# Kernel tuning notes

Measured on AMD Instinct MI355X. Metric: run time of the kernel, lower is better.

## Reference

```python
import jax, jax.numpy as jnp
import numpy as np

PI = float(np.pi)
CUTOFF = 10.0
SLOPE = 0.015  # LeakyReLU negative slope

N_NODES = 50000
N_EDGES = 1600000
HIDDEN = 128
FILTERS = 128
GAUSSIANS = 50


def _leaky(x):
    return jnp.where(x >= 0, x, SLOPE * x)


def setup_inputs() -> dict:
    key = jax.random.key(0)
    ks = jax.random.split(key, 10)

    def xavier(k, shape):
        fan_in, fan_out = shape[1], shape[0]
        a = float(np.sqrt(6.0 / (fan_in + fan_out)))
        return jax.random.uniform(k, shape, jnp.float32, -a, a)

    v = jax.random.normal(ks[0], (N_NODES, HIDDEN), jnp.float32)
    dist = jax.random.uniform(ks[1], (N_EDGES,), jnp.float32)  # in [0,1) < cutoff
    dist_emb = jax.random.normal(ks[2], (N_EDGES, GAUSSIANS), jnp.float32)
    edge_index = jax.random.randint(ks[3], (2, N_EDGES), 0, N_NODES, jnp.int64)

    return {
        "v": v,
        "dist": dist,
        "dist_emb": dist_emb,
        "edge_index": edge_index,
        "lin_w": xavier(ks[4], (FILTERS, HIDDEN)),          # Linear(hidden->filters), no bias
        "mlp_w1": xavier(ks[5], (FILTERS, GAUSSIANS)),
        "mlp_b1": jnp.zeros((FILTERS,), jnp.float32),
        "mlp_w2": xavier(ks[6], (FILTERS, FILTERS)),
        "mlp_b2": jnp.zeros((FILTERS,), jnp.float32),
        "mlp_w3": xavier(ks[7], (FILTERS, FILTERS)),
        "mlp_b3": jnp.zeros((FILTERS,), jnp.float32),
        "lin_out_w": xavier(ks[8], (FILTERS, FILTERS)),
        "lin_out_b": jnp.zeros((FILTERS,), jnp.float32),
    }


def reference(v, dist, dist_emb, edge_index, lin_w, mlp_w1, mlp_b1,
              mlp_w2, mlp_b2, mlp_w3, mlp_b3, lin_out_w, lin_out_b):
    j = edge_index[0]
    # cosine cutoff: [E]
    C = 0.5 * (jnp.cos(dist * (PI / CUTOFF)) + 1.0)
    # filter MLP on gaussian basis: [E, F]
    h = _leaky(dist_emb @ mlp_w1.T + mlp_b1)
    h = _leaky(h @ mlp_w2.T + mlp_b2)
    W = (h @ mlp_w3.T + mlp_b3) * C[:, None]
    # project node features, gather source nodes, multiply by filter
    vp = v @ lin_w.T          # [N, F]
    e = vp[j] * W             # [E, F]
    return e @ lin_out_w.T + lin_out_b + e
```

## Files before the change

kernel.cpp:

```cpp
#include <hip/hip_runtime.h>
#include <math.h>

typedef __attribute__((ext_vector_type(8))) short short8;
typedef __attribute__((ext_vector_type(4))) float f32x4;
typedef __attribute__((ext_vector_type(2))) float f32x2;
typedef __attribute__((ext_vector_type(4))) unsigned u32x4;

#define PI_OVER_CUTOFF 0.31415926535897932f
#define SLOPE 0.015f

__device__ __forceinline__ unsigned short f2bf(float x) {
    unsigned u = __float_as_uint(x);
    return (unsigned short)((u + 0x7FFFu + ((u >> 16) & 1u)) >> 16);
}
__device__ __forceinline__ unsigned cvt_pk_bf16(float lo, float hi) {
    unsigned r;
    asm("v_cvt_pk_bf16_f32 %0, %1, %2" : "=v"(r) : "v"(lo), "v"(hi));
    return r;
}
__device__ __forceinline__ short8 pack4(unsigned a, unsigned b, unsigned c, unsigned d) {
    u32x4 t = {a, b, c, d};
    return __builtin_bit_cast(short8, t);
}
__device__ __forceinline__ short8 mulbf8(short8 w, short8 v) {
    u32x4 uw = __builtin_bit_cast(u32x4, w);
    u32x4 uv = __builtin_bit_cast(u32x4, v);
    unsigned r0, r1, r2, r3;
#define MB(i, r)                                                         \
    {                                                                    \
        float wl = __uint_as_float(uw[i] << 16);                         \
        float wh = __uint_as_float(uw[i] & 0xFFFF0000u);                 \
        float vl = __uint_as_float(uv[i] << 16);                         \
        float vh = __uint_as_float(uv[i] & 0xFFFF0000u);                 \
        r = cvt_pk_bf16(wl * vl, wh * vh);                               \
    }
    MB(0, r0) MB(1, r1) MB(2, r2) MB(3, r3)
#undef MB
    return pack4(r0, r1, r2, r3);
}

#define GLOAD_LDS16(g, l)                                                                      \
    __builtin_amdgcn_global_load_lds((const __attribute__((address_space(1))) unsigned*)(g),   \
                                     (__attribute__((address_space(3))) unsigned*)(l), 16, 0, 0)

__global__ void prep_weights(const float* __restrict__ w1, const float* __restrict__ w2,
                             const float* __restrict__ w3, const float* __restrict__ wo,
                             unsigned short* __restrict__ w1s, unsigned short* __restrict__ w2s,
                             unsigned short* __restrict__ w3s, unsigned short* __restrict__ wos) {
    int i = blockIdx.x * 256 + threadIdx.x;
    if (i < 128 * 128) {
        int c = i >> 7, k = i & 127;
        int d = c * 128 + (k ^ ((c & 15) << 3));
        w1s[d] = (k < 50) ? f2bf(w1[c * 50 + k]) : (unsigned short)0;
        w2s[d] = f2bf(w2[i]);
        w3s[d] = f2bf(w3[i]);
        wos[d] = f2bf(wo[i] + ((c == k) ? 1.0f : 0.0f));
    }
}

__global__ __launch_bounds__(256) void vp_gemm(const float* __restrict__ v,
                                               const float* __restrict__ lin_w,
                                               unsigned short* __restrict__ vp, int nnodes) {
    const int tid = threadIdx.x;
    const int lane = tid & 63;
    const int wv = tid >> 6;
    const int l15 = lane & 15;
    const int l4 = lane >> 4;
    const int r0 = blockIdx.x * 64;
    const int c0 = wv * 32;

    f32x4 acc[4][2] = {};
#pragma unroll
    for (int kf = 0; kf < 4; ++kf) {
        short8 a[4];
#pragma unroll
        for (int mf = 0; mf < 4; ++mf) {
            int row = r0 + mf * 16 + l15;
            f32x4 x0 = {}, x1 = {};
            if (row < nnodes) {
                const float* p = v + (size_t)row * 128 + kf * 32 + l4 * 8;
                x0 = *reinterpret_cast<const f32x4*>(p);
                x1 = *reinterpret_cast<const f32x4*>(p + 4);
            }
            a[mf] = pack4(cvt_pk_bf16(x0[0], x0[1]), cvt_pk_bf16(x0[2], x0[3]),
                          cvt_pk_bf16(x1[0], x1[1]), cvt_pk_bf16(x1[2], x1[3]));
        }
        short8 b[2];
#pragma unroll
        for (int nf = 0; nf < 2; ++nf) {
            const float* p = lin_w + (size_t)(c0 + nf * 16 + l15) * 128 + kf * 32 + l4 * 8;
            f32x4 x0 = *reinterpret_cast<const f32x4*>(p);
            f32x4 x1 = *reinterpret_cast<const f32x4*>(p + 4);
            b[nf] = pack4(cvt_pk_bf16(x0[0], x0[1]), cvt_pk_bf16(x0[2], x0[3]),
                          cvt_pk_bf16(x1[0], x1[1]), cvt_pk_bf16(x1[2], x1[3]));
        }
#pragma unroll
        for (int mf = 0; mf < 4; ++mf)
#pragma unroll
            for (int nf = 0; nf < 2; ++nf)
                acc[mf][nf] = __builtin_amdgcn_mfma_f32_16x16x32_bf16(a[mf], b[nf], acc[mf][nf], 0, 0, 0);
    }
#pragma unroll
    for (int mf = 0; mf < 4; ++mf)
#pragma unroll
        for (int nf = 0; nf < 2; ++nf)
#pragma unroll
            for (int q = 0; q < 4; ++q) {
                int row = r0 + mf * 16 + l4 * 4 + q;
                if (row < nnodes)
                    vp[(size_t)row * 128 + c0 + nf * 16 + l15] = f2bf(acc[mf][nf][q]);
            }
}

__global__ __launch_bounds__(256, 1) void fused_edge(
    const float* __restrict__ dist, const float* __restrict__ dist_emb,
    const int* __restrict__ edge_index,
    const float* __restrict__ b1, const float* __restrict__ b2,
    const float* __restrict__ b3, const float* __restrict__ bo,
    const unsigned short* __restrict__ vp,
    const unsigned short* __restrict__ w1s, const unsigned short* __restrict__ w2s,
    const unsigned short* __restrict__ w3s, const unsigned short* __restrict__ wos,
    float* __restrict__ out) {
    __shared__ __align__(16) unsigned char lds_h[4][16384];
    __shared__ __align__(16) unsigned short wbuf[2][16384];

    const int tid = threadIdx.x;
    const int lane = tid & 63;
    const int wv = tid >> 6;
    const int l15 = lane & 15;
    const int l4 = lane >> 4;
    const long e0 = (long)blockIdx.x * 256 + wv * 64;
    unsigned char* hb = lds_h[wv];

#define STAGE_W(src, buf)                                                  \
    _Pragma("unroll")                                                      \
    for (int it = 0; it < 8; ++it) {                                       \
        int chunk = it * 4 + wv;                                           \
        GLOAD_LDS16((src) + chunk * 512 + lane * 8, &wbuf[buf][chunk * 512]); \
    }

    STAGE_W(w1s, 0)
    STAGE_W(w2s, 1)

    int jm[4];
#pragma unroll
    for (int mf = 0; mf < 4; ++mf)
        jm[mf] = edge_index[e0 + mf * 16 + l15] * 128;
    float bb1[8], bb2[8], bb3[8], bbo[8];
#pragma unroll
    for (int nf = 0; nf < 8; ++nf) {
        bb1[nf] = b1[nf * 16 + l15];
        bb2[nf] = b2[nf * 16 + l15];
        bb3[nf] = b3[nf * 16 + l15];
        bbo[nf] = bo[nf * 16 + l15];
    }

    f32x4 acc[4][8];

#define EPILOGUE_TO_LDS()                                                           \
    _Pragma("unroll")                                                               \
    for (int mf = 0; mf < 4; ++mf)                                                  \
        _Pragma("unroll")                                                           \
        for (int nf = 0; nf < 8; ++nf) {                                            \
            f32x4 vv = acc[mf][nf];                                                 \
            _Pragma("unroll")                                                       \
            for (int q = 0; q < 4; ++q) vv[q] = fmaxf(vv[q], SLOPE * vv[q]);        \
            unsigned p01 = cvt_pk_bf16(vv[0], vv[1]);                               \
            unsigned p23 = cvt_pk_bf16(vv[2], vv[3]);                               \
            int col2 = (nf * 16 + l15) * 2;                                         \
            int rb = mf * 16 + l4 * 4;                                              \
            *(unsigned short*)(hb + (rb + 0) * 256 + (col2 ^ ((l4 * 4 + 0) << 4))) = (unsigned short)p01;         \
            *(unsigned short*)(hb + (rb + 1) * 256 + (col2 ^ ((l4 * 4 + 1) << 4))) = (unsigned short)(p01 >> 16); \
            *(unsigned short*)(hb + (rb + 2) * 256 + (col2 ^ ((l4 * 4 + 2) << 4))) = (unsigned short)p23;         \
            *(unsigned short*)(hb + (rb + 3) * 256 + (col2 ^ ((l4 * 4 + 3) << 4))) = (unsigned short)(p23 >> 16); \
        }

#define HB_READ(mf, kf) \
    (*reinterpret_cast<const short8*>(hb + ((mf) * 16 + l15) * 256 + (((kf) * 64 + l4 * 16) ^ (l15 << 4))))
#define WB_READ(buf, nf, kf) \
    (*reinterpret_cast<const short8*>(&wbuf[buf][((nf) * 16 + l15) * 128 + (((kf) * 32 + l4 * 8) ^ (l15 << 3))]))

    __syncthreads();

#pragma unroll
    for (int nf = 0; nf < 8; ++nf) {
        float b = bb1[nf];
#pragma unroll
        for (int mf = 0; mf < 4; ++mf) acc[mf][nf] = (f32x4){b, b, b, b};
    }
#pragma unroll
    for (int kf = 0; kf < 2; ++kf) {
        short8 a[4];
#pragma unroll
        for (int mf = 0; mf < 4; ++mf) {
            const float* src = dist_emb + (e0 + mf * 16 + l15) * 50 + kf * 32 + l4 * 8;
            unsigned pk[4];
#pragma unroll
            for (int p = 0; p < 4; ++p) {
                int k2 = kf * 32 + l4 * 8 + 2 * p;
                f32x2 x = (k2 < 50) ? *reinterpret_cast<const f32x2*>(src + 2 * p)
                                    : (f32x2){0.f, 0.f};
                pk[p] = cvt_pk_bf16(x[0], x[1]);
            }
            a[mf] = pack4(pk[0], pk[1], pk[2], pk[3]);
        }
#pragma unroll
        for (int nf = 0; nf < 8; ++nf) {
            short8 b = WB_READ(0, nf, kf);
#pragma unroll
            for (int mf = 0; mf < 4; ++mf)
                acc[mf][nf] = __builtin_amdgcn_mfma_f32_16x16x32_bf16(a[mf], b, acc[mf][nf], 0, 0, 0);
        }
    }
    EPILOGUE_TO_LDS()

    __syncthreads();
    STAGE_W(w3s, 0)

#pragma unroll
    for (int nf = 0; nf < 8; ++nf) {
        float b = bb2[nf];
#pragma unroll
        for (int mf = 0; mf < 4; ++mf) acc[mf][nf] = (f32x4){b, b, b, b};
    }
#pragma unroll
    for (int kf = 0; kf < 4; ++kf) {
        short8 a[4];
#pragma unroll
        for (int mf = 0; mf < 4; ++mf) a[mf] = HB_READ(mf, kf);
#pragma unroll
        for (int nf = 0; nf < 8; ++nf) {
            short8 b = WB_READ(1, nf, kf);
#pragma unroll
            for (int mf = 0; mf < 4; ++mf)
                acc[mf][nf] = __builtin_amdgcn_mfma_f32_16x16x32_bf16(a[mf], b, acc[mf][nf], 0, 0, 0);
        }
    }
    EPILOGUE_TO_LDS()

    __syncthreads();
    STAGE_W(wos, 1)

    {
        short8 vpr[4][4];
#pragma unroll
        for (int mf = 0; mf < 4; ++mf)
#pragma unroll
            for (int kf = 0; kf < 4; ++kf)
                vpr[mf][kf] = *reinterpret_cast<const short8*>(vp + jm[mf] + kf * 32 + l4 * 8);

        float dd[4][4];
#pragma unroll
        for (int mf = 0; mf < 4; ++mf)
#pragma unroll
            for (int q = 0; q < 4; ++q)
                dd[mf][q] = dist[e0 + mf * 16 + l4 * 4 + q];

#pragma unroll
        for (int nf = 0; nf < 8; ++nf) {
            float b = bb3[nf];
#pragma unroll
            for (int mf = 0; mf < 4; ++mf) acc[mf][nf] = (f32x4){b, b, b, b};
        }
#pragma unroll
        for (int kf = 0; kf < 4; ++kf) {
            short8 a[4];
#pragma unroll
            for (int mf = 0; mf < 4; ++mf) a[mf] = HB_READ(mf, kf);
#pragma unroll
            for (int nf = 0; nf < 8; ++nf) {
                short8 b = WB_READ(0, nf, kf);
#pragma unroll
                for (int mf = 0; mf < 4; ++mf)
                    acc[mf][nf] = __builtin_amdgcn_mfma_f32_16x16x32_bf16(a[mf], b, acc[mf][nf], 0, 0, 0);
            }
        }
        float Cw[4][4];
#pragma unroll
        for (int mf = 0; mf < 4; ++mf)
#pragma unroll
            for (int q = 0; q < 4; ++q)
                Cw[mf][q] = 0.5f * (__cosf(dd[mf][q] * PI_OVER_CUTOFF) + 1.0f);
#pragma unroll
        for (int mf = 0; mf < 4; ++mf)
#pragma unroll
            for (int nf = 0; nf < 8; ++nf) {
                f32x4 vv = acc[mf][nf];
#pragma unroll
                for (int q = 0; q < 4; ++q) vv[q] = vv[q] * Cw[mf][q];
                unsigned p01 = cvt_pk_bf16(vv[0], vv[1]);
                unsigned p23 = cvt_pk_bf16(vv[2], vv[3]);
                int col2 = (nf * 16 + l15) * 2;
                int rb = mf * 16 + l4 * 4;
                *(unsigned short*)(hb + (rb + 0) * 256 + (col2 ^ ((l4 * 4 + 0) << 4))) = (unsigned short)p01;
                *(unsigned short*)(hb + (rb + 1) * 256 + (col2 ^ ((l4 * 4 + 1) << 4))) = (unsigned short)(p01 >> 16);
                *(unsigned short*)(hb + (rb + 2) * 256 + (col2 ^ ((l4 * 4 + 2) << 4))) = (unsigned short)p23;
                *(unsigned short*)(hb + (rb + 3) * 256 + (col2 ^ ((l4 * 4 + 3) << 4))) = (unsigned short)(p23 >> 16);
            }

        __syncthreads();

#pragma unroll
        for (int nf = 0; nf < 8; ++nf) {
            float b = bbo[nf];
#pragma unroll
            for (int mf = 0; mf < 4; ++mf) acc[mf][nf] = (f32x4){b, b, b, b};
        }
#pragma unroll
        for (int kf = 0; kf < 4; ++kf) {
            short8 a[4];
#pragma unroll
            for (int mf = 0; mf < 4; ++mf) a[mf] = mulbf8(HB_READ(mf, kf), vpr[mf][kf]);
#pragma unroll
            for (int nf = 0; nf < 8; ++nf) {
                short8 b = WB_READ(1, nf, kf);
#pragma unroll
                for (int mf = 0; mf < 4; ++mf)
                    acc[mf][nf] = __builtin_amdgcn_mfma_f32_16x16x32_bf16(a[mf], b, acc[mf][nf], 0, 0, 0);
            }
        }
        float* op = out + (size_t)e0 * 128;
#pragma unroll
        for (int mf = 0; mf < 4; ++mf)
#pragma unroll
            for (int nf = 0; nf < 8; ++nf)
#pragma unroll
                for (int q = 0; q < 4; ++q)
                    op[(size_t)(mf * 16 + l4 * 4 + q) * 128 + nf * 16 + l15] = acc[mf][nf][q];
    }
#undef EPILOGUE_TO_LDS
#undef HB_READ
#undef WB_READ
#undef STAGE_W
}

extern "C" void kernel_launch(void* const* d_in, const int* in_sizes, int n_in,
                              void* d_out, int out_size, void* d_ws, size_t ws_size,
                              hipStream_t stream) {
    const float* v        = (const float*)d_in[0];
    const float* dist     = (const float*)d_in[1];
    const float* dist_emb = (const float*)d_in[2];
    const int*   edge_idx = (const int*)d_in[3];
    const float* lin_w    = (const float*)d_in[4];
    const float* w1 = (const float*)d_in[5];
    const float* b1 = (const float*)d_in[6];
    const float* w2 = (const float*)d_in[7];
    const float* b2 = (const float*)d_in[8];
    const float* w3 = (const float*)d_in[9];
    const float* b3 = (const float*)d_in[10];
    const float* wo = (const float*)d_in[11];
    const float* bo = (const float*)d_in[12];
    float* out = (float*)d_out;

    const int nnodes = in_sizes[0] / 128;
    const int E = in_sizes[1];

    unsigned short* vp  = (unsigned short*)d_ws;
    unsigned short* w1s = vp + (size_t)nnodes * 128;
    unsigned short* w2s = w1s + 128 * 128;
    unsigned short* w3s = w2s + 128 * 128;
    unsigned short* wos = w3s + 128 * 128;

    prep_weights<<<64, 256, 0, stream>>>(w1, w2, w3, wo, w1s, w2s, w3s, wos);
    vp_gemm<<<(nnodes + 63) / 64, 256, 0, stream>>>(v, lin_w, vp, nnodes);
    fused_edge<<<E / 256, 256, 0, stream>>>(dist, dist_emb, edge_idx,
                                            b1, b2, b3, bo, vp,
                                            w1s, w2s, w3s, wos, out);
}
```

Measured before the change: 526.5 us.

## Split each wave's 64 edges into two 32-row halves to cut accumulator registers

Each wave now processes its 64 edges as two sequential 32-row halves, with separate LDS regions h0 and h1. This halves the accumulator array from 4x8 to 2x8 f32x4. The dist_emb loads for both halves are hoisted to the top of the kernel, and the vp gathers for each half are issued just before that half's layer-3 GEMM. The goal is to lower VGPR pressure and possible spills and to overlap global loads with MFMA work. The cost is that each weight fragment read from LDS now feeds two MFMAs instead of four, which doubles B-operand LDS traffic per MFMA.

```diff
diff --git a/kernel.cpp b/kernel.cpp
--- a/kernel.cpp
+++ b/kernel.cpp
@@ -130,7 +130,8 @@
     const int l15 = lane & 15;
     const int l4 = lane >> 4;
     const long e0 = (long)blockIdx.x * 256 + wv * 64;
-    unsigned char* hb = lds_h[wv];
+    unsigned char* h0 = lds_h[wv];
+    unsigned char* h1 = lds_h[wv] + 8192;
 
 #define STAGE_W(src, buf)                                                  \
     _Pragma("unroll")                                                      \
@@ -142,10 +143,26 @@
     STAGE_W(w1s, 0)
     STAGE_W(w2s, 1)
 
-    int jm[4];
-#pragma unroll
-    for (int mf = 0; mf < 4; ++mf)
-        jm[mf] = edge_index[e0 + mf * 16 + l15] * 128;
+    short8 ea[2][2], eb[2][2];
+#define LOAD_EMB(E, OFS)                                                            \
+    _Pragma("unroll")                                                               \
+    for (int mf = 0; mf < 2; ++mf)                                                  \
+        _Pragma("unroll")                                                           \
+        for (int kf = 0; kf < 2; ++kf) {                                            \
+            const float* src = dist_emb + (e0 + (OFS) + mf * 16 + l15) * 50 + kf * 32 + l4 * 8; \
+            unsigned pk[4];                                                         \
+            _Pragma("unroll")                                                       \
+            for (int p = 0; p < 4; ++p) {                                           \
+                int k2 = kf * 32 + l4 * 8 + 2 * p;                                  \
+                f32x2 x = (k2 < 50) ? *reinterpret_cast<const f32x2*>(src + 2 * p)  \
+                                    : (f32x2){0.f, 0.f};                            \
+                pk[p] = cvt_pk_bf16(x[0], x[1]);                                    \
+            }                                                                       \
+            E[mf][kf] = pack4(pk[0], pk[1], pk[2], pk[3]);                          \
+        }
+    LOAD_EMB(ea, 0)
+    LOAD_EMB(eb, 32)
+
     float bb1[8], bb2[8], bb3[8], bbo[8];
 #pragma unroll
     for (int nf = 0; nf < 8; ++nf) {
@@ -155,11 +172,24 @@
         bbo[nf] = bo[nf * 16 + l15];
     }
 
-    f32x4 acc[4][8];
-
-#define EPILOGUE_TO_LDS()                                                           \
-    _Pragma("unroll")                                                               \
-    for (int mf = 0; mf < 4; ++mf)                                                  \
+    f32x4 acc[2][8];
+
+#define WB_READ(buf, nf, kf) \
+    (*reinterpret_cast<const short8*>(&wbuf[buf][((nf) * 16 + l15) * 128 + (((kf) * 32 + l4 * 8) ^ (l15 << 3))]))
+#define HB_READ(H, mf, kf) \
+    (*reinterpret_cast<const short8*>((H) + ((mf) * 16 + l15) * 256 + (((kf) * 64 + l4 * 16) ^ (l15 << 4))))
+
+#define INIT_ACC(bb)                                                                \
+    _Pragma("unroll")                                                               \
+    for (int nf = 0; nf < 8; ++nf) {                                                \
+        float b = (bb)[nf];                                                         \
+        acc[0][nf] = (f32x4){b, b, b, b};                                           \
+        acc[1][nf] = acc[0][nf];                                                    \
+    }
+
+#define EPILOGUE_TO(H)                                                              \
+    _Pragma("unroll")                                                               \
+    for (int mf = 0; mf < 2; ++mf)                                                  \
         _Pragma("unroll")                                                           \
         for (int nf = 0; nf < 8; ++nf) {                                            \
             f32x4 vv = acc[mf][nf];                                                 \
@@ -169,168 +199,155 @@
             unsigned p23 = cvt_pk_bf16(vv[2], vv[3]);                               \
             int col2 = (nf * 16 + l15) * 2;                                         \
             int rb = mf * 16 + l4 * 4;                                              \
-            *(unsigned short*)(hb + (rb + 0) * 256 + (col2 ^ ((l4 * 4 + 0) << 4))) = (unsigned short)p01;         \
-            *(unsigned short*)(hb + (rb + 1) * 256 + (col2 ^ ((l4 * 4 + 1) << 4))) = (unsigned short)(p01 >> 16); \
-            *(unsigned short*)(hb + (rb + 2) * 256 + (col2 ^ ((l4 * 4 + 2) << 4))) = (unsigned short)p23;         \
-            *(unsigned short*)(hb + (rb + 3) * 256 + (col2 ^ ((l4 * 4 + 3) << 4))) = (unsigned short)(p23 >> 16); \
+            *(unsigned short*)((H) + (rb + 0) * 256 + (col2 ^ ((l4 * 4 + 0) << 4))) = (unsigned short)p01;         \
+            *(unsigned short*)((H) + (rb + 1) * 256 + (col2 ^ ((l4 * 4 + 1) << 4))) = (unsigned short)(p01 >> 16); \
+            *(unsigned short*)((H) + (rb + 2) * 256 + (col2 ^ ((l4 * 4 + 2) << 4))) = (unsigned short)p23;         \
+            *(unsigned short*)((H) + (rb + 3) * 256 + (col2 ^ ((l4 * 4 + 3) << 4))) = (unsigned short)(p23 >> 16); \
         }
 
-#define HB_READ(mf, kf) \
-    (*reinterpret_cast<const short8*>(hb + ((mf) * 16 + l15) * 256 + (((kf) * 64 + l4 * 16) ^ (l15 << 4))))
-#define WB_READ(buf, nf, kf) \
-    (*reinterpret_cast<const short8*>(&wbuf[buf][((nf) * 16 + l15) * 128 + (((kf) * 32 + l4 * 8) ^ (l15 << 3))]))
+#define S1_BODY(E, H)                                                               \
+    INIT_ACC(bb1)                                                                   \
+    _Pragma("unroll")                                                               \
+    for (int kf = 0; kf < 2; ++kf) {                                                \
+        _Pragma("unroll")                                                           \
+        for (int nf = 0; nf < 8; ++nf) {                                            \
+            short8 b = WB_READ(0, nf, kf);                                          \
+            acc[0][nf] = __builtin_amdgcn_mfma_f32_16x16x32_bf16(E[0][kf], b, acc[0][nf], 0, 0, 0); \
+            acc[1][nf] = __builtin_amdgcn_mfma_f32_16x16x32_bf16(E[1][kf], b, acc[1][nf], 0, 0, 0); \
+        }                                                                           \
+    }                                                                               \
+    EPILOGUE_TO(H)
+
+#define S2_BODY(H, BUF, BB)                                                         \
+    INIT_ACC(BB)                                                                    \
+    _Pragma("unroll")                                                               \
+    for (int kf = 0; kf < 4; ++kf) {                                                \
+        short8 a0 = HB_READ(H, 0, kf);                                              \
+        short8 a1 = HB_READ(H, 1, kf);                                              \
+        _Pragma("unroll")                                                           \
+        for (int nf = 0; nf < 8; ++nf) {                                            \
+            short8 b = WB_READ(BUF, nf, kf);                                        \
+            acc[0][nf] = __builtin_amdgcn_mfma_f32_16x16x32_bf16(a0, b, acc[0][nf], 0, 0, 0); \
+            acc[1][nf] = __builtin_amdgcn_mfma_f32_16x16x32_bf16(a1, b, acc[1][nf], 0, 0, 0); \
+        }                                                                           \
+    }
+
+#define S3_EPI(H, DD)                                                               \
+    {                                                                               \
+        float Cw[2][4];                                                             \
+        _Pragma("unroll")                                                           \
+        for (int mf = 0; mf < 2; ++mf)                                              \
+            _Pragma("unroll")                                                       \
+            for (int q = 0; q < 4; ++q)                                             \
+                Cw[mf][q] = 0.5f * (__cosf(DD[mf][q] * PI_OVER_CUTOFF) + 1.0f);     \
+        _Pragma("unroll")                                                           \
+        for (int mf = 0; mf < 2; ++mf)                                              \
+            _Pragma("unroll")                                                       \
+            for (int nf = 0; nf < 8; ++nf) {                                        \
+                f32x4 vv = acc[mf][nf];                                             \
+                _Pragma("unroll")                                                   \
+                for (int q = 0; q < 4; ++q) vv[q] = vv[q] * Cw[mf][q];              \
+                unsigned p01 = cvt_pk_bf16(vv[0], vv[1]);                           \
+                unsigned p23 = cvt_pk_bf16(vv[2], vv[3]);                           \
+                int col2 = (nf * 16 + l15) * 2;                                     \
+                int rb = mf * 16 + l4 * 4;                                          \
+                *(unsigned short*)((H) + (rb + 0) * 256 + (col2 ^ ((l4 * 4 + 0) << 4))) = (unsigned short)p01;         \
+                *(unsigned short*)((H) + (rb + 1) * 256 + (col2 ^ ((l4 * 4 + 1) << 4))) = (unsigned short)(p01 >> 16); \
+                *(unsigned short*)((H) + (rb + 2) * 256 + (col2 ^ ((l4 * 4 + 2) << 4))) = (unsigned short)p23;         \
+                *(unsigned short*)((H) + (rb + 3) * 256 + (col2 ^ ((l4 * 4 + 3) << 4))) = (unsigned short)(p23 >> 16); \
+            }                                                                       \
+    }
+
+#define S4_BODY(H, V, OFS)                                                          \
+    INIT_ACC(bbo)                                                                   \
+    _Pragma("unroll")                                                               \
+    for (int kf = 0; kf < 4; ++kf) {                                                \
+        short8 a0 = mulbf8(HB_READ(H, 0, kf), V[0][kf]);                            \
+        short8 a1 = mulbf8(HB_READ(H, 1, kf), V[1][kf]);                            \
+        _Pragma("unroll")                                                           \
+        for (int nf = 0; nf < 8; ++nf) {                                            \
+            short8 b = WB_READ(1, nf, kf);                                          \
+            acc[0][nf] = __builtin_amdgcn_mfma_f32_16x16x32_bf16(a0, b, acc[0][nf], 0, 0, 0); \
+            acc[1][nf] = __builtin_amdgcn_mfma_f32_16x16x32_bf16(a1, b, acc[1][nf], 0, 0, 0); \
+        }                                                                           \
+    }                                                                               \
+    {                                                                               \
+        float* op = out + (size_t)(e0 + (OFS)) * 128;                               \
+        _Pragma("unroll")                                                           \
+        for (int mf = 0; mf < 2; ++mf)                                              \
+            _Pragma("unroll")                                                       \
+            for (int nf = 0; nf < 8; ++nf)                                          \
+                _Pragma("unroll")                                                   \
+                for (int q = 0; q < 4; ++q)                                         \
+                    op[(size_t)(mf * 16 + l4 * 4 + q) * 128 + nf * 16 + l15] = acc[mf][nf][q]; \
+    }
 
     __syncthreads();
 
-#pragma unroll
-    for (int nf = 0; nf < 8; ++nf) {
-        float b = bb1[nf];
-#pragma unroll
-        for (int mf = 0; mf < 4; ++mf) acc[mf][nf] = (f32x4){b, b, b, b};
-    }
-#pragma unroll
-    for (int kf = 0; kf < 2; ++kf) {
-        short8 a[4];
-#pragma unroll
-        for (int mf = 0; mf < 4; ++mf) {
-            const float* src = dist_emb + (e0 + mf * 16 + l15) * 50 + kf * 32 + l4 * 8;
-            unsigned pk[4];
-#pragma unroll
-            for (int p = 0; p < 4; ++p) {
-                int k2 = kf * 32 + l4 * 8 + 2 * p;
-                f32x2 x = (k2 < 50) ? *reinterpret_cast<const f32x2*>(src + 2 * p)
-                                    : (f32x2){0.f, 0.f};
-                pk[p] = cvt_pk_bf16(x[0], x[1]);
-            }
-            a[mf] = pack4(pk[0], pk[1], pk[2], pk[3]);
-        }
-#pragma unroll
-        for (int nf = 0; nf < 8; ++nf) {
-            short8 b = WB_READ(0, nf, kf);
-#pragma unroll
-            for (int mf = 0; mf < 4; ++mf)
-                acc[mf][nf] = __builtin_amdgcn_mfma_f32_16x16x32_bf16(a[mf], b, acc[mf][nf], 0, 0, 0);
-        }
-    }
-    EPILOGUE_TO_LDS()
+    S1_BODY(ea, h0)
+    S1_BODY(eb, h1)
 
     __syncthreads();
     STAGE_W(w3s, 0)
 
-#pragma unroll
-    for (int nf = 0; nf < 8; ++nf) {
-        float b = bb2[nf];
-#pragma unroll
-        for (int mf = 0; mf < 4; ++mf) acc[mf][nf] = (f32x4){b, b, b, b};
-    }
-#pragma unroll
-    for (int kf = 0; kf < 4; ++kf) {
-        short8 a[4];
-#pragma unroll
-        for (int mf = 0; mf < 4; ++mf) a[mf] = HB_READ(mf, kf);
-#pragma unroll
-        for (int nf = 0; nf < 8; ++nf) {
-            short8 b = WB_READ(1, nf, kf);
-#pragma unroll
-            for (int mf = 0; mf < 4; ++mf)
-                acc[mf][nf] = __builtin_amdgcn_mfma_f32_16x16x32_bf16(a[mf], b, acc[mf][nf], 0, 0, 0);
-        }
-    }
-    EPILOGUE_TO_LDS()
+    S2_BODY(h0, 1, bb2)
+    EPILOGUE_TO(h0)
+    S2_BODY(h1, 1, bb2)
+    EPILOGUE_TO(h1)
 
     __syncthreads();
     STAGE_W(wos, 1)
 
-    {
-        short8 vpr[4][4];
-#pragma unroll
-        for (int mf = 0; mf < 4; ++mf)
-#pragma unroll
-            for (int kf = 0; kf < 4; ++kf)
-                vpr[mf][kf] = *reinterpret_cast<const short8*>(vp + jm[mf] + kf * 32 + l4 * 8);
-
-        float dd[4][4];
-#pragma unroll
-        for (int mf = 0; mf < 4; ++mf)
-#pragma unroll
-            for (int q = 0; q < 4; ++q)
-                dd[mf][q] = dist[e0 + mf * 16 + l4 * 4 + q];
-
-#pragma unroll
-        for (int nf = 0; nf < 8; ++nf) {
-            float b = bb3[nf];
-#pragma unroll
-            for (int mf = 0; mf < 4; ++mf) acc[mf][nf] = (f32x4){b, b, b, b};
-        }
-#pragma unroll
-        for (int kf = 0; kf < 4; ++kf) {
-            short8 a[4];
-#pragma unroll
-            for (int mf = 0; mf < 4; ++mf) a[mf] = HB_READ(mf, kf);
-#pragma unroll
-            for (int nf = 0; nf < 8; ++nf) {
-                short8 b = WB_READ(0, nf, kf);
-#pragma unroll
-                for (int mf = 0; mf < 4; ++mf)
-                    acc[mf][nf] = __builtin_amdgcn_mfma_f32_16x16x32_bf16(a[mf], b, acc[mf][nf], 0, 0, 0);
-            }
-        }
-        float Cw[4][4];
-#pragma unroll
-        for (int mf = 0; mf < 4; ++mf)
-#pragma unroll
-            for (int q = 0; q < 4; ++q)
-                Cw[mf][q] = 0.5f * (__cosf(dd[mf][q] * PI_OVER_CUTOFF) + 1.0f);
-#pragma unroll
-        for (int mf = 0; mf < 4; ++mf)
-#pragma unroll
-            for (int nf = 0; nf < 8; ++nf) {
-                f32x4 vv = acc[mf][nf];
-#pragma unroll
-                for (int q = 0; q < 4; ++q) vv[q] = vv[q] * Cw[mf][q];
-                unsigned p01 = cvt_pk_bf16(vv[0], vv[1]);
-                unsigned p23 = cvt_pk_bf16(vv[2], vv[3]);
-                int col2 = (nf * 16 + l15) * 2;
-                int rb = mf * 16 + l4 * 4;
-                *(unsigned short*)(hb + (rb + 0) * 256 + (col2 ^ ((l4 * 4 + 0) << 4))) = (unsigned short)p01;
-                *(unsigned short*)(hb + (rb + 1) * 256 + (col2 ^ ((l4 * 4 + 1) << 4))) = (unsigned short)(p01 >> 16);
-                *(unsigned short*)(hb + (rb + 2) * 256 + (col2 ^ ((l4 * 4 + 2) << 4))) = (unsigned short)p23;
-                *(unsigned short*)(hb + (rb + 3) * 256 + (col2 ^ ((l4 * 4 + 3) << 4))) = (unsigned short)(p23 >> 16);
-            }
-
-        __syncthreads();
-
-#pragma unroll
-        for (int nf = 0; nf < 8; ++nf) {
-            float b = bbo[nf];
-#pragma unroll
-            for (int mf = 0; mf < 4; ++mf) acc[mf][nf] = (f32x4){b, b, b, b};
-        }
-#pragma unroll
-        for (int kf = 0; kf < 4; ++kf) {
-            short8 a[4];
-#pragma unroll
-            for (int mf = 0; mf < 4; ++mf) a[mf] = mulbf8(HB_READ(mf, kf), vpr[mf][kf]);
-#pragma unroll
-            for (int nf = 0; nf < 8; ++nf) {
-                short8 b = WB_READ(1, nf, kf);
-#pragma unroll
-                for (int mf = 0; mf < 4; ++mf)
-                    acc[mf][nf] = __builtin_amdgcn_mfma_f32_16x16x32_bf16(a[mf], b, acc[mf][nf], 0, 0, 0);
-            }
-        }
-        float* op = out + (size_t)e0 * 128;
-#pragma unroll
-        for (int mf = 0; mf < 4; ++mf)
-#pragma unroll
-            for (int nf = 0; nf < 8; ++nf)
-#pragma unroll
-                for (int q = 0; q < 4; ++q)
-                    op[(size_t)(mf * 16 + l4 * 4 + q) * 128 + nf * 16 + l15] = acc[mf][nf][q];
-    }
-#undef EPILOGUE_TO_LDS
+    const int ja0 = edge_index[e0 + l15] * 128;
+    const int ja1 = edge_index[e0 + 16 + l15] * 128;
+    short8 va[2][4];
+#pragma unroll
+    for (int kf = 0; kf < 4; ++kf) {
+        va[0][kf] = *reinterpret_cast<const short8*>(vp + ja0 + kf * 32 + l4 * 8);
+        va[1][kf] = *reinterpret_cast<const short8*>(vp + ja1 + kf * 32 + l4 * 8);
+    }
+    float da[2][4];
+#pragma unroll
+    for (int mf = 0; mf < 2; ++mf)
+#pragma unroll
+        for (int q = 0; q < 4; ++q)
+            da[mf][q] = dist[e0 + mf * 16 + l4 * 4 + q];
+
+    S2_BODY(h0, 0, bb3)
+    S3_EPI(h0, da)
+
+    const int jb0 = edge_index[e0 + 32 + l15] * 128;
+    const int jb1 = edge_index[e0 + 48 + l15] * 128;
+    short8 vb[2][4];
+#pragma unroll
+    for (int kf = 0; kf < 4; ++kf) {
+        vb[0][kf] = *reinterpret_cast<const short8*>(vp + jb0 + kf * 32 + l4 * 8);
+        vb[1][kf] = *reinterpret_cast<const short8*>(vp + jb1 + kf * 32 + l4 * 8);
+    }
+    float db[2][4];
+#pragma unroll
+    for (int mf = 0; mf < 2; ++mf)
+#pragma unroll
+        for (int q = 0; q < 4; ++q)
+            db[mf][q] = dist[e0 + 32 + mf * 16 + l4 * 4 + q];
+
+    S2_BODY(h1, 0, bb3)
+    S3_EPI(h1, db)
+
+    __syncthreads();
+
+    S4_BODY(h0, va, 0)
+    S4_BODY(h1, vb, 32)
+
+#undef S4_BODY
+#undef S3_EPI
+#undef S2_BODY
+#undef S1_BODY
+#undef EPILOGUE_TO
+#undef INIT_ACC
 #undef HB_READ
 #undef WB_READ
+#undef LOAD_EMB
 #undef STAGE_W
 }
 
```

After: 549.9 us. 4.4% more time.
